# Optimization experiments

Hardware: AMD Instinct MI355X
Metric: run time of the kernel (lower is better)

Reference implementation:

```python
import jax, jax.numpy as jnp
import numpy as np
from jax import lax

N = 1024
N_I = 64
N_AV = 10
ALPHA = 0.5
RHO = 0.9
GAMMA = 1.0


def _make_params(seed=0):
    rng = np.random.RandomState(seed)
    diluition = 1.0 - N_AV / N
    W = rng.uniform(-1, 1, [N, N])
    W = W * (rng.uniform(0, 1, [N, N]) > diluition)
    eig = np.linalg.eigvals(W)
    W = (RHO * W / np.max(np.absolute(eig))).astype(np.float32)
    # N_i != 1 branch: gaussian input weights scaled by gamma
    W_in = (GAMMA * rng.randn(N_I, N)).astype(np.float32)
    return jnp.asarray(W), jnp.asarray(W_in)


def setup_inputs() -> dict:
    key = jax.random.key(0)
    Input = jax.random.normal(key, (128, N_I, 512), dtype=jnp.float32)
    W, W_in = _make_params()
    return {"Input": Input, "W": W, "W_in": W_in}


def reference(Input, W, W_in):
    # Input: [B, N_i, T] -> X: [B, N, T]
    B = Input.shape[0]
    x0 = jnp.zeros((B, W.shape[0]), dtype=Input.dtype)
    seq = jnp.transpose(Input, (2, 0, 1))  # [T, B, N_i]

    def step(x, s):
        x = (1.0 - ALPHA) * x + ALPHA * jnp.tanh(s @ W_in + x @ W)
        return x, x

    _, X = lax.scan(step, x0, seq)  # [T, B, N]
    return jnp.transpose(X, (1, 2, 0))  # [B, N, T]
```

## Files before the change

### kernel.cpp

```cpp
#include <hip/hip_runtime.h>
#include <hip/hip_fp16.h>
#include <cstdint>
#include <cstddef>

#define BB 128
#define NN 1024
#define NI 64
#define TT 512
#define MAXNNZ 16384
#define NE 28
#define TH 16

#define WS_OFFS   0u
#define WS_IDX    16384u
#define WS_VAL    65536u
#define WS_PERM   131072u
#define WS_IPERM  135168u
#define WS_XSTATE 139264u
#define WS_WINP   663552u
#define WS_EIDX2  925696u
#define WS_CNT16  983040u
#define WS_OFF16  1048576u
#define WS_U      1114112u
#define WS_U2     (WS_U + 67108864u)

__global__ __launch_bounds__(64) void k_count16(const float* __restrict__ W, int* __restrict__ cnt16) {
    int bc = blockIdx.x;
    int s = bc & 15, g = bc >> 4;
    int col = g * 64 + threadIdx.x;
    int c = 0;
    for (int q = 0; q < 64; ++q) {
        int k = s * 64 + q;
        c += (W[(size_t)k * NN + col] != 0.0f) ? 1 : 0;
    }
    cnt16[col * 16 + s] = c;
}

__global__ __launch_bounds__(1024) void k_scanrank(const int* __restrict__ cnt16,
        int* __restrict__ offs, int* __restrict__ off16,
        int* __restrict__ perm, int* __restrict__ iperm) {
    __shared__ int s[NN];
    int n = threadIdx.x;
    int t = 0;
#pragma unroll
    for (int q = 0; q < 16; ++q) t += cnt16[n * 16 + q];
    s[n] = t;
    __syncthreads();
    for (int d = 1; d < NN; d <<= 1) {
        int v = (n >= d) ? s[n - d] : 0;
        __syncthreads();
        s[n] += v;
        __syncthreads();
    }
    int incl = s[n];
    offs[n + 1] = (incl < MAXNNZ) ? incl : MAXNNZ;
    if (n == 0) offs[0] = 0;
    int base = incl - t;
#pragma unroll
    for (int q = 0; q < 16; ++q) {
        off16[n * 16 + q] = base;
        base += cnt16[n * 16 + q];
    }
    __syncthreads();
    int myc = t;
    s[n] = myc;
    __syncthreads();
    int r = 0;
    for (int m = 0; m < NN; ++m) {
        int cm = s[m];
        r += (cm > myc || (cm == myc && m < n)) ? 1 : 0;
    }
    perm[r] = n;
    iperm[n] = r;
}

__global__ __launch_bounds__(1024) void k_choice2(const int* __restrict__ offs,
        const unsigned short* __restrict__ gidx, const int* __restrict__ perm,
        const int* __restrict__ iperm, unsigned short* __restrict__ eidx2) {
    __shared__ unsigned short rk[NN][NE];
    __shared__ unsigned short scnt[NN];
    __shared__ unsigned char ctr8[896][32];
    int n = threadIdx.x;
    {
        int rr = n;
        int c = perm[rr];
        int o0 = offs[c];
        int cn = offs[c + 1] - o0;
        if (cn > NE) cn = NE;
        scnt[rr] = (unsigned short)cn;
        for (int j = 0; j < cn; ++j) rk[rr][j] = (unsigned short)iperm[(int)gidx[o0 + j]];
    }
    __syncthreads();
    int tid = n;
    if (tid < 896) {
        int task = tid >> 1, h = tid & 1;
        int w = task / NE, j = task % NE;
        unsigned char* mc = &ctr8[tid][0];
        for (int b = 0; b < 32; ++b) mc[b] = 0;
        unsigned sel = 0u;
        for (int l = 0; l < 32; ++l) {
            int rr = 64 * w + 32 * h + l;
            if (j < (int)scnt[rr]) {
                int rv = (int)rk[rr][j];
                int bA = rv & 31, bB = (rv ^ (rv >> 5)) & 31;
                if (mc[bA] <= mc[bB]) mc[bA]++;
                else { sel |= (1u << l); mc[bB]++; }
            }
        }
        for (int sweep = 0; sweep < 12; ++sweep) {
            bool ch = false;
            for (int l = 0; l < 32; ++l) {
                int rr = 64 * w + 32 * h + l;
                if (j < (int)scnt[rr]) {
                    int rv = (int)rk[rr][j];
                    int bA = rv & 31, bB = (rv ^ (rv >> 5)) & 31;
                    int isB = (int)((sel >> l) & 1u);
                    int cur = isB ? bB : bA, alt = isB ? bA : bB;
                    if ((int)mc[cur] > (int)mc[alt] + 1) {
                        mc[cur]--; mc[alt]++;
                        sel ^= (1u << l);
                        ch = true;
                    }
                }
            }
            if (!ch) break;
        }
        for (int l = 0; l < 32; ++l) {
            int rr = 64 * w + 32 * h + l;
            if (j < (int)scnt[rr]) {
                int rv = (int)rk[rr][j];
                int bB = (rv ^ (rv >> 5)) & 31;
                int addr = ((sel >> l) & 1u) ? (4096 + (((rv & ~31) | bB) << 2))
                                             : (rv << 2);
                eidx2[j * NN + rr] = (unsigned short)addr;
            }
        }
        int minb = 0, minl = (int)mc[0];
        for (int b = 1; b < 32; ++b)
            if ((int)mc[b] < minl) { minl = (int)mc[b]; minb = b; }
        unsigned short pad = (unsigned short)(minb << 2);
        for (int l = 0; l < 32; ++l) {
            int rr = 64 * w + 32 * h + l;
            if (j >= (int)scnt[rr]) eidx2[j * NN + rr] = pad;
        }
    }
}

__global__ __launch_bounds__(64) void k_fill16(const float* __restrict__ W, const int* __restrict__ off16,
                                               unsigned short* __restrict__ idx, float* __restrict__ val) {
    int bc = blockIdx.x;
    int s = bc & 15, g = bc >> 4;
    int col = g * 64 + threadIdx.x;
    int p = off16[col * 16 + s];
    for (int q = 0; q < 64; ++q) {
        int k = s * 64 + q;
        float w = W[(size_t)k * NN + col];
        if (w != 0.0f) { idx[p] = (unsigned short)k; val[p] = w; ++p; }
    }
}

__global__ __launch_bounds__(256) void k_permwin(const float* __restrict__ Win, const int* __restrict__ perm,
                                                 float* __restrict__ Winp) {
    int idx = blockIdx.x * 256 + threadIdx.x;
    int i = idx >> 10, r = idx & 1023;
    Winp[idx] = Win[(i << 10) + perm[r]];
}

__global__ __launch_bounds__(256) void k_uproj3(const float* __restrict__ In, const float* __restrict__ Winp,
                                                __half* __restrict__ U, int t0c, int nblk) {
    int b  = blockIdx.x / nblk;
    int tq = blockIdx.x % nblk;
    int t0 = t0c + tq * 32;
    __shared__ float s[32][NI + 1];
    int tid = threadIdx.x;
    {
        int i = tid >> 2, g = tid & 3;
        const float* ip = In + ((size_t)b * NI + i) * TT + t0 + g * 8;
        float4 v0 = *(const float4*)(ip);
        float4 v1 = *(const float4*)(ip + 4);
        s[g * 8 + 0][i] = v0.x; s[g * 8 + 1][i] = v0.y;
        s[g * 8 + 2][i] = v0.z; s[g * 8 + 3][i] = v0.w;
        s[g * 8 + 4][i] = v1.x; s[g * 8 + 5][i] = v1.y;
        s[g * 8 + 6][i] = v1.z; s[g * 8 + 7][i] = v1.w;
    }
    __syncthreads();
    const float4* W4 = (const float4*)Winp;
    uint2* U2 = (uint2*)U;
    for (int th = 0; th < 2; ++th) {
        float4 acc[16];
#pragma unroll
        for (int t = 0; t < 16; ++t) acc[t] = make_float4(0.f, 0.f, 0.f, 0.f);
        for (int i = 0; i < NI; ++i) {
            float4 w = W4[(size_t)i * 256 + tid];
#pragma unroll
            for (int t = 0; t < 16; ++t) {
                float sv = s[th * 16 + t][i];
                acc[t].x = fmaf(w.x, sv, acc[t].x);
                acc[t].y = fmaf(w.y, sv, acc[t].y);
                acc[t].z = fmaf(w.z, sv, acc[t].z);
                acc[t].w = fmaf(w.w, sv, acc[t].w);
            }
        }
#pragma unroll
        for (int t = 0; t < 16; ++t) {
            __half2 h01 = __floats2half2_rn(acc[t].x, acc[t].y);
            __half2 h23 = __floats2half2_rn(acc[t].z, acc[t].w);
            uint2 pk;
            pk.x = *(unsigned int*)&h01;
            pk.y = *(unsigned int*)&h23;
            U2[((size_t)(tq * 32 + th * 16 + t) * BB + b) * 256 + tid] = pk;
        }
    }
}

__device__ __forceinline__ float fast_tanh(float z) {
    float a = fabsf(z) * 2.885390082f;
    a = fminf(a, 60.0f);
    float e = __builtin_amdgcn_exp2f(a);
    float r = 1.0f - __fdividef(2.0f, e + 1.0f);
    return z < 0.0f ? -r : r;
}

#define L28(M) \
  M(0) M(1) M(2) M(3) M(4) M(5) M(6) M(7) M(8) M(9) M(10) M(11) M(12) M(13) \
  M(14) M(15) M(16) M(17) M(18) M(19) M(20) M(21) M(22) M(23) M(24) M(25) M(26) M(27)

#define DW(i)  float w##i; int a##i;
#define IW(i)  { a##i = (int)eidx2[(i) * NN + n]; \
                 w##i = (cnt > i) ? gval[o0 + i] : 0.0f; }

#define PIN_ALL \
  asm volatile("" : "+v"(w0),"+v"(w1),"+v"(w2),"+v"(w3),"+v"(w4),"+v"(w5),"+v"(w6),"+v"(w7)); \
  asm volatile("" : "+v"(w8),"+v"(w9),"+v"(w10),"+v"(w11),"+v"(w12),"+v"(w13),"+v"(w14),"+v"(w15)); \
  asm volatile("" : "+v"(w16),"+v"(w17),"+v"(w18),"+v"(w19),"+v"(w20),"+v"(w21),"+v"(w22),"+v"(w23)); \
  asm volatile("" : "+v"(w24),"+v"(w25),"+v"(w26),"+v"(w27)); \
  asm volatile("" : "+v"(a0),"+v"(a1),"+v"(a2),"+v"(a3),"+v"(a4),"+v"(a5),"+v"(a6),"+v"(a7)); \
  asm volatile("" : "+v"(a8),"+v"(a9),"+v"(a10),"+v"(a11),"+v"(a12),"+v"(a13),"+v"(a14),"+v"(a15)); \
  asm volatile("" : "+v"(a16),"+v"(a17),"+v"(a18),"+v"(a19),"+v"(a20),"+v"(a21),"+v"(a22),"+v"(a23)); \
  asm volatile("" : "+v"(a24),"+v"(a25),"+v"(a26),"+v"(a27));

#define GRP(J, i0, i1, i2, i3) \
  if ((J) < wmax) { \
    float q0 = *(const float*)(xp + a##i0); \
    float q1 = *(const float*)(xp + a##i1); \
    float q2 = *(const float*)(xp + a##i2); \
    float q3 = *(const float*)(xp + a##i3); \
    z0 = fmaf(w##i0, q0, z0); z1 = fmaf(w##i1, q1, z1); \
    z2 = fmaf(w##i2, q2, z2); z3 = fmaf(w##i3, q3, z3); \
  }

#define GATHER_ALL \
  GRP(0, 0,1,2,3)      GRP(4, 4,5,6,7)      GRP(8, 8,9,10,11) \
  GRP(12, 12,13,14,15) GRP(16, 16,17,18,19) GRP(20, 20,21,22,23) \
  GRP(24, 24,25,26,27)

#define STEP(PH, XDST) { \
    float u = un1; un1 = un2; \
    int tn = t + 2; tn = (tn < Tc) ? tn : (Tc - 1); \
    un2 = (float)Ub[(size_t)tn * ustep]; \
    const char* xp = xb + (PH); \
    float z0 = u, z1 = 0.f, z2 = 0.f, z3 = 0.f; \
    GATHER_ALL \
    x = 0.5f * x + 0.5f * fast_tanh((z0 + z1) + (z2 + z3)); \
    XDST = x; \
    float* wb = (float*)(xb + ((PH) ^ 8192)); \
    wb[n] = x; \
    wb[NN + nB] = x; \
    __syncthreads(); \
    ++t; \
}

__global__ __launch_bounds__(1024, 4)
void k_fused(const __half* __restrict__ Uread, __half* __restrict__ Uwrite,
             const float* __restrict__ In, const float* __restrict__ Winp,
             const int* __restrict__ offs, const unsigned short* __restrict__ eidx2,
             const float* __restrict__ gval, const int* __restrict__ perm,
             float* __restrict__ out, float* __restrict__ xstate,
             int t0r, int Tc, int t0u, int Tcu) {
    __shared__ float smem[4 * 32 * 65];
    int tid = threadIdx.x;
    if (blockIdx.x < BB) {
        int b = blockIdx.x, n = tid;
        int c = perm[n];
        int nB = (n & ~31) | ((n ^ (n >> 5)) & 31);
        int o0 = offs[c];
        int cnt = offs[c + 1] - o0;
        L28(DW)
        L28(IW)
        PIN_ALL
        int wmax = cnt;
#pragma unroll
        for (int d = 1; d < 64; d <<= 1) {
            int o = __shfl_xor(wmax, d);
            wmax = wmax > o ? wmax : o;
        }
        wmax = __builtin_amdgcn_readfirstlane(wmax);

        float x = (t0r == 0) ? 0.0f : xstate[((size_t)b << 10) + n];
        smem[n] = x;
        smem[NN + nB] = x;
        __syncthreads();

        char* xb = (char*)&smem[0];
        const __half* Ub = Uread + (size_t)b * NN + n;
        const size_t ustep = (size_t)BB * NN;
        float un1 = (float)Ub[0];
        float un2 = (float)Ub[(size_t)((1 < Tc) ? 1 : 0) * ustep];

        for (int tb = 0; tb < Tc; tb += TH) {
            PIN_ALL
            int t = tb;
            float y0, y1, y2, y3, y4, y5, y6, y7, y8, y9, y10, y11, y12, y13, y14, y15;
            STEP(0,    y0)
            STEP(8192, y1)
            STEP(0,    y2)
            STEP(8192, y3)
            STEP(0,    y4)
            STEP(8192, y5)
            STEP(0,    y6)
            STEP(8192, y7)
            STEP(0,    y8)
            STEP(8192, y9)
            STEP(0,    y10)
            STEP(8192, y11)
            STEP(0,    y12)
            STEP(8192, y13)
            STEP(0,    y14)
            STEP(8192, y15)
            float4* op = (float4*)(out + ((size_t)b * NN + c) * TT + (size_t)(t0r + tb));
            op[0] = make_float4(y0,  y1,  y2,  y3);
            op[1] = make_float4(y4,  y5,  y6,  y7);
            op[2] = make_float4(y8,  y9,  y10, y11);
            op[3] = make_float4(y12, y13, y14, y15);
        }
        if (t0r + Tc < TT) xstate[((size_t)b << 10) + n] = x;
    } else {
        if (Tcu <= 0) return;
        int b = blockIdx.x - BB;
        int sub = tid >> 8, stid = tid & 255;
        float* sg = smem + sub * 32 * 65;
        const float4* W4 = (const float4*)Winp;
        uint2* U2w = (uint2*)Uwrite;
        int ntile = Tcu >> 5;
        int nrep = (ntile + 3) >> 2;
        for (int rep = 0; rep < nrep; ++rep) {
            int tq = rep * 4 + sub;
            bool act = tq < ntile;
            int tg = t0u + tq * 32;
            __syncthreads();
            if (act) {
                int i = stid >> 2, g4 = stid & 3;
                const float* ip = In + ((size_t)b * NI + i) * TT + tg + g4 * 8;
                float4 v0 = *(const float4*)(ip);
                float4 v1 = *(const float4*)(ip + 4);
                sg[(g4 * 8 + 0) * 65 + i] = v0.x; sg[(g4 * 8 + 1) * 65 + i] = v0.y;
                sg[(g4 * 8 + 2) * 65 + i] = v0.z; sg[(g4 * 8 + 3) * 65 + i] = v0.w;
                sg[(g4 * 8 + 4) * 65 + i] = v1.x; sg[(g4 * 8 + 5) * 65 + i] = v1.y;
                sg[(g4 * 8 + 6) * 65 + i] = v1.z; sg[(g4 * 8 + 7) * 65 + i] = v1.w;
            }
            __syncthreads();
            if (act) {
                for (int th = 0; th < 2; ++th) {
                    float4 acc[16];
#pragma unroll
                    for (int t = 0; t < 16; ++t) acc[t] = make_float4(0.f, 0.f, 0.f, 0.f);
                    for (int i = 0; i < NI; ++i) {
                        float4 w = W4[(size_t)i * 256 + stid];
#pragma unroll
                        for (int t = 0; t < 16; ++t) {
                            float sv = sg[(th * 16 + t) * 65 + i];
                            acc[t].x = fmaf(w.x, sv, acc[t].x);
                            acc[t].y = fmaf(w.y, sv, acc[t].y);
                            acc[t].z = fmaf(w.z, sv, acc[t].z);
                            acc[t].w = fmaf(w.w, sv, acc[t].w);
                        }
                    }
#pragma unroll
                    for (int t = 0; t < 16; ++t) {
                        __half2 h01 = __floats2half2_rn(acc[t].x, acc[t].y);
                        __half2 h23 = __floats2half2_rn(acc[t].z, acc[t].w);
                        uint2 pk;
                        pk.x = *(unsigned int*)&h01;
                        pk.y = *(unsigned int*)&h23;
                        U2w[((size_t)(tq * 32 + th * 16 + t) * BB + b) * 256 + stid] = pk;
                    }
                }
            }
        }
    }
}

extern "C" void kernel_launch(void* const* d_in, const int* in_sizes, int n_in,
                              void* d_out, int out_size, void* d_ws, size_t ws_size,
                              hipStream_t stream) {
    const float* In  = (const float*)d_in[0];
    const float* W   = (const float*)d_in[1];
    const float* Win = (const float*)d_in[2];
    float* out = (float*)d_out;
    char* ws = (char*)d_ws;
    int* offs           = (int*)(ws + WS_OFFS);
    unsigned short* idx = (unsigned short*)(ws + WS_IDX);
    float* val          = (float*)(ws + WS_VAL);
    int* perm           = (int*)(ws + WS_PERM);
    int* iperm          = (int*)(ws + WS_IPERM);
    float* xstate       = (float*)(ws + WS_XSTATE);
    float* Winp         = (float*)(ws + WS_WINP);
    unsigned short* eidx2 = (unsigned short*)(ws + WS_EIDX2);
    int* cnt16          = (int*)(ws + WS_CNT16);
    int* off16          = (int*)(ws + WS_OFF16);
    __half* U0          = (__half*)(ws + WS_U);
    __half* U1          = (__half*)(ws + WS_U2);

    k_count16<<<256, 64, 0, stream>>>(W, cnt16);
    k_scanrank<<<1, 1024, 0, stream>>>(cnt16, offs, off16, perm, iperm);
    k_fill16<<<256, 64, 0, stream>>>(W, off16, idx, val);
    k_choice2<<<1, 1024, 0, stream>>>(offs, idx, perm, iperm, eidx2);
    k_permwin<<<256, 256, 0, stream>>>(Win, perm, Winp);

    if ((size_t)WS_U2 + (size_t)256 * BB * NN * 2 <= ws_size) {
        k_uproj3<<<BB, 256, 0, stream>>>(In, Winp, U0, 0, 1);
        k_fused<<<2 * BB, 1024, 0, stream>>>(U0, U1, In, Winp, offs, eidx2, val, perm,
                                             out, xstate, 0, 32, 32, 64);
        k_fused<<<2 * BB, 1024, 0, stream>>>(U1, U0, In, Winp, offs, eidx2, val, perm,
                                             out, xstate, 32, 64, 96, 128);
        k_fused<<<2 * BB, 1024, 0, stream>>>(U0, U1, In, Winp, offs, eidx2, val, perm,
                                             out, xstate, 96, 128, 224, 256);
        k_fused<<<2 * BB, 1024, 0, stream>>>(U1, U0, In, Winp, offs, eidx2, val, perm,
                                             out, xstate, 224, 256, 480, 32);
        k_fused<<<BB, 1024, 0, stream>>>(U0, U0, In, Winp, offs, eidx2, val, perm,
                                         out, xstate, 480, 32, TT, 0);
    } else {
        for (int t0 = 0; t0 < TT; t0 += 128) {
            k_uproj3<<<BB * 4, 256, 0, stream>>>(In, Winp, U0, t0, 4);
            k_fused<<<BB, 1024, 0, stream>>>(U0, U0, In, Winp, offs, eidx2, val, perm,
                                             out, xstate, t0, 128, TT, 0);
        }
    }
}
```

Baseline: 568.3 us.

## Replace multi-launch ping-pong with single persistent producer/consumer kernel using flags

Replaces the chain of five fused launches, which alternated between two U buffers, with one persistent kernel. Half the blocks compute the input projection U per 32-step tile and publish a per-batch, per-tile flag with release semantics; the other half run the recurrence, spin-waiting on each flag with acquire loads. This removes the launch boundaries and the chunked schedule, so projection and recurrence overlap continuously. It needs a full-length U buffer and relies on both block kinds being co-resident, so the spin-wait carries deadlock and occupancy risk, and the occupancy hint drops to 2 blocks per SM.

```diff
diff --git a/kernel.cpp b/kernel.cpp
--- a/kernel.cpp
+++ b/kernel.cpp
@@ -22,7 +22,6 @@
 #define WS_CNT16  983040u
 #define WS_OFF16  1048576u
 #define WS_U      1114112u
-#define WS_U2     (WS_U + 67108864u)
 
 __global__ __launch_bounds__(64) void k_count16(const float* __restrict__ W, int* __restrict__ cnt16) {
     int bc = blockIdx.x;
@@ -164,6 +163,223 @@
     int idx = blockIdx.x * 256 + threadIdx.x;
     int i = idx >> 10, r = idx & 1023;
     Winp[idx] = Win[(i << 10) + perm[r]];
+}
+
+__device__ __forceinline__ float fast_tanh(float z) {
+    float a = fabsf(z) * 2.885390082f;
+    a = fminf(a, 60.0f);
+    float e = __builtin_amdgcn_exp2f(a);
+    float r = 1.0f - __fdividef(2.0f, e + 1.0f);
+    return z < 0.0f ? -r : r;
+}
+
+#define L28(M) \
+  M(0) M(1) M(2) M(3) M(4) M(5) M(6) M(7) M(8) M(9) M(10) M(11) M(12) M(13) \
+  M(14) M(15) M(16) M(17) M(18) M(19) M(20) M(21) M(22) M(23) M(24) M(25) M(26) M(27)
+
+#define DW(i)  float w##i; int a##i;
+#define IW(i)  { a##i = (int)eidx2[(i) * NN + n]; \
+                 w##i = (cnt > i) ? gval[o0 + i] : 0.0f; }
+
+#define PIN_ALL \
+  asm volatile("" : "+v"(w0),"+v"(w1),"+v"(w2),"+v"(w3),"+v"(w4),"+v"(w5),"+v"(w6),"+v"(w7)); \
+  asm volatile("" : "+v"(w8),"+v"(w9),"+v"(w10),"+v"(w11),"+v"(w12),"+v"(w13),"+v"(w14),"+v"(w15)); \
+  asm volatile("" : "+v"(w16),"+v"(w17),"+v"(w18),"+v"(w19),"+v"(w20),"+v"(w21),"+v"(w22),"+v"(w23)); \
+  asm volatile("" : "+v"(w24),"+v"(w25),"+v"(w26),"+v"(w27)); \
+  asm volatile("" : "+v"(a0),"+v"(a1),"+v"(a2),"+v"(a3),"+v"(a4),"+v"(a5),"+v"(a6),"+v"(a7)); \
+  asm volatile("" : "+v"(a8),"+v"(a9),"+v"(a10),"+v"(a11),"+v"(a12),"+v"(a13),"+v"(a14),"+v"(a15)); \
+  asm volatile("" : "+v"(a16),"+v"(a17),"+v"(a18),"+v"(a19),"+v"(a20),"+v"(a21),"+v"(a22),"+v"(a23)); \
+  asm volatile("" : "+v"(a24),"+v"(a25),"+v"(a26),"+v"(a27));
+
+#define GRP(J, i0, i1, i2, i3) \
+  if ((J) < wmax) { \
+    float q0 = *(const float*)(xp + a##i0); \
+    float q1 = *(const float*)(xp + a##i1); \
+    float q2 = *(const float*)(xp + a##i2); \
+    float q3 = *(const float*)(xp + a##i3); \
+    z0 = fmaf(w##i0, q0, z0); z1 = fmaf(w##i1, q1, z1); \
+    z2 = fmaf(w##i2, q2, z2); z3 = fmaf(w##i3, q3, z3); \
+  }
+
+#define GATHER_ALL \
+  GRP(0, 0,1,2,3)      GRP(4, 4,5,6,7)      GRP(8, 8,9,10,11) \
+  GRP(12, 12,13,14,15) GRP(16, 16,17,18,19) GRP(20, 20,21,22,23) \
+  GRP(24, 24,25,26,27)
+
+#define STEPX(PH, XDST) { \
+    float u = un1; un1 = un2; \
+    int tn = t + 2; tn = (tn < tlim) ? tn : tlim; \
+    un2 = (float)Ub[(size_t)tn * ustep]; \
+    const char* xp = xb + (PH); \
+    float z0 = u, z1 = 0.f, z2 = 0.f, z3 = 0.f; \
+    GATHER_ALL \
+    x = 0.5f * x + 0.5f * fast_tanh((z0 + z1) + (z2 + z3)); \
+    XDST = x; \
+    float* wb = (float*)(xb + ((PH) ^ 8192)); \
+    wb[n] = x; \
+    wb[NN + nB] = x; \
+    __syncthreads(); \
+    ++t; \
+}
+
+#define REC16 \
+    PIN_ALL \
+    int t = tb; \
+    float y0, y1, y2, y3, y4, y5, y6, y7, y8, y9, y10, y11, y12, y13, y14, y15; \
+    STEPX(0,    y0)  STEPX(8192, y1)  STEPX(0,    y2)  STEPX(8192, y3) \
+    STEPX(0,    y4)  STEPX(8192, y5)  STEPX(0,    y6)  STEPX(8192, y7) \
+    STEPX(0,    y8)  STEPX(8192, y9)  STEPX(0,    y10) STEPX(8192, y11) \
+    STEPX(0,    y12) STEPX(8192, y13) STEPX(0,    y14) STEPX(8192, y15)
+
+__global__ __launch_bounds__(1024, 2)
+void k_pipe(const float* __restrict__ In, const float* __restrict__ Winp,
+            __half* __restrict__ U,
+            const int* __restrict__ offs, const unsigned short* __restrict__ eidx2,
+            const float* __restrict__ gval, const int* __restrict__ perm,
+            float* __restrict__ out, int* __restrict__ flags) {
+    __shared__ float smem[4096];
+    int tid = threadIdx.x;
+    if (blockIdx.x < BB) {
+        int b = blockIdx.x, n = tid;
+        int c = perm[n];
+        int nB = (n & ~31) | ((n ^ (n >> 5)) & 31);
+        int o0 = offs[c];
+        int cnt = offs[c + 1] - o0;
+        L28(DW)
+        L28(IW)
+        PIN_ALL
+        int wmax = cnt;
+#pragma unroll
+        for (int d = 1; d < 64; d <<= 1) {
+            int o = __shfl_xor(wmax, d);
+            wmax = wmax > o ? wmax : o;
+        }
+        wmax = __builtin_amdgcn_readfirstlane(wmax);
+
+        float x = 0.0f;
+        smem[n] = 0.0f;
+        smem[NN + nB] = 0.0f;
+        __syncthreads();
+
+        char* xb = (char*)&smem[0];
+        const __half* Ub = U + (size_t)b * NN + n;
+        const size_t ustep = (size_t)BB * NN;
+
+        for (int tile = 0; tile < 16; ++tile) {
+            if (tid == 0) {
+                while (__hip_atomic_load(&flags[b * 16 + tile], __ATOMIC_ACQUIRE,
+                                         __HIP_MEMORY_SCOPE_AGENT) == 0) {
+                    __builtin_amdgcn_s_sleep(2);
+                }
+            }
+            __syncthreads();
+            int tlim = 32 * tile + 31;
+            float un1 = (float)Ub[(size_t)(32 * tile) * ustep];
+            float un2 = (float)Ub[(size_t)(32 * tile + 1) * ustep];
+            for (int tb = 32 * tile; tb < 32 * tile + 32; tb += TH) {
+                REC16
+                float4* op = (float4*)(out + ((size_t)b * NN + c) * TT + (size_t)tb);
+                op[0] = make_float4(y0,  y1,  y2,  y3);
+                op[1] = make_float4(y4,  y5,  y6,  y7);
+                op[2] = make_float4(y8,  y9,  y10, y11);
+                op[3] = make_float4(y12, y13, y14, y15);
+            }
+        }
+    } else {
+        int b = blockIdx.x - BB;
+        int n4 = tid & 255;
+        int tl = (tid >> 8) * 8;
+        const float4* W4 = (const float4*)Winp;
+        uint2* U2w = (uint2*)U;
+        for (int tq = 0; tq < 16; ++tq) {
+            int tg = tq * 32;
+            if (tid < 512) {
+                int i = tid >> 3, g4 = tid & 7;
+                float4 v = *(const float4*)(In + ((size_t)b * NI + i) * TT + tg + g4 * 4);
+                *(float4*)&smem[i * 40 + g4 * 4] = v;
+            }
+            __syncthreads();
+            float4 a0 = {0,0,0,0}, a1 = {0,0,0,0}, a2 = {0,0,0,0}, a3 = {0,0,0,0};
+            float4 a4 = {0,0,0,0}, a5 = {0,0,0,0}, a6 = {0,0,0,0}, a7 = {0,0,0,0};
+            for (int i = 0; i < NI; ++i) {
+                float4 w = W4[(size_t)i * 256 + n4];
+                float4 sa = *(const float4*)&smem[i * 40 + tl];
+                float4 sb = *(const float4*)&smem[i * 40 + tl + 4];
+                a0.x = fmaf(w.x, sa.x, a0.x); a0.y = fmaf(w.y, sa.x, a0.y);
+                a0.z = fmaf(w.z, sa.x, a0.z); a0.w = fmaf(w.w, sa.x, a0.w);
+                a1.x = fmaf(w.x, sa.y, a1.x); a1.y = fmaf(w.y, sa.y, a1.y);
+                a1.z = fmaf(w.z, sa.y, a1.z); a1.w = fmaf(w.w, sa.y, a1.w);
+                a2.x = fmaf(w.x, sa.z, a2.x); a2.y = fmaf(w.y, sa.z, a2.y);
+                a2.z = fmaf(w.z, sa.z, a2.z); a2.w = fmaf(w.w, sa.z, a2.w);
+                a3.x = fmaf(w.x, sa.w, a3.x); a3.y = fmaf(w.y, sa.w, a3.y);
+                a3.z = fmaf(w.z, sa.w, a3.z); a3.w = fmaf(w.w, sa.w, a3.w);
+                a4.x = fmaf(w.x, sb.x, a4.x); a4.y = fmaf(w.y, sb.x, a4.y);
+                a4.z = fmaf(w.z, sb.x, a4.z); a4.w = fmaf(w.w, sb.x, a4.w);
+                a5.x = fmaf(w.x, sb.y, a5.x); a5.y = fmaf(w.y, sb.y, a5.y);
+                a5.z = fmaf(w.z, sb.y, a5.z); a5.w = fmaf(w.w, sb.y, a5.w);
+                a6.x = fmaf(w.x, sb.z, a6.x); a6.y = fmaf(w.y, sb.z, a6.y);
+                a6.z = fmaf(w.z, sb.z, a6.z); a6.w = fmaf(w.w, sb.z, a6.w);
+                a7.x = fmaf(w.x, sb.w, a7.x); a7.y = fmaf(w.y, sb.w, a7.y);
+                a7.z = fmaf(w.z, sb.w, a7.z); a7.w = fmaf(w.w, sb.w, a7.w);
+            }
+#define PSTORE(J, AJ) { \
+            int tt = tg + tl + (J); \
+            __half2 h01 = __floats2half2_rn(AJ.x, AJ.y); \
+            __half2 h23 = __floats2half2_rn(AJ.z, AJ.w); \
+            uint2 pk; pk.x = *(unsigned int*)&h01; pk.y = *(unsigned int*)&h23; \
+            U2w[((size_t)tt * BB + b) * 256 + n4] = pk; }
+            PSTORE(0, a0) PSTORE(1, a1) PSTORE(2, a2) PSTORE(3, a3)
+            PSTORE(4, a4) PSTORE(5, a5) PSTORE(6, a6) PSTORE(7, a7)
+#undef PSTORE
+            __syncthreads();
+            if (tid == 0) {
+                __hip_atomic_store(&flags[b * 16 + tq], 1, __ATOMIC_RELEASE,
+                                   __HIP_MEMORY_SCOPE_AGENT);
+            }
+        }
+    }
+}
+
+__global__ __launch_bounds__(1024, 4)
+void k_rec(const __half* __restrict__ U,
+           const int* __restrict__ offs, const unsigned short* __restrict__ eidx2,
+           const float* __restrict__ gval, const int* __restrict__ perm,
+           float* __restrict__ out, float* __restrict__ xstate, int t0r, int Tc) {
+    __shared__ float smem[4096];
+    int b = blockIdx.x, n = threadIdx.x;
+    int c = perm[n];
+    int nB = (n & ~31) | ((n ^ (n >> 5)) & 31);
+    int o0 = offs[c];
+    int cnt = offs[c + 1] - o0;
+    L28(DW)
+    L28(IW)
+    PIN_ALL
+    int wmax = cnt;
+#pragma unroll
+    for (int d = 1; d < 64; d <<= 1) {
+        int o = __shfl_xor(wmax, d);
+        wmax = wmax > o ? wmax : o;
+    }
+    wmax = __builtin_amdgcn_readfirstlane(wmax);
+    float x = (t0r == 0) ? 0.0f : xstate[((size_t)b << 10) + n];
+    smem[n] = x;
+    smem[NN + nB] = x;
+    __syncthreads();
+    char* xb = (char*)&smem[0];
+    const __half* Ub = U + (size_t)b * NN + n;
+    const size_t ustep = (size_t)BB * NN;
+    int tlim = Tc - 1;
+    float un1 = (float)Ub[0];
+    float un2 = (float)Ub[(size_t)((1 < Tc) ? 1 : 0) * ustep];
+    for (int tb = 0; tb < Tc; tb += TH) {
+        REC16
+        float4* op = (float4*)(out + ((size_t)b * NN + c) * TT + (size_t)(t0r + tb));
+        op[0] = make_float4(y0,  y1,  y2,  y3);
+        op[1] = make_float4(y4,  y5,  y6,  y7);
+        op[2] = make_float4(y8,  y9,  y10, y11);
+        op[3] = make_float4(y12, y13, y14, y15);
+    }
+    if (t0r + Tc < TT) xstate[((size_t)b << 10) + n] = x;
 }
 
 __global__ __launch_bounds__(256) void k_uproj3(const float* __restrict__ In, const float* __restrict__ Winp,
@@ -209,183 +425,6 @@
             pk.x = *(unsigned int*)&h01;
             pk.y = *(unsigned int*)&h23;
             U2[((size_t)(tq * 32 + th * 16 + t) * BB + b) * 256 + tid] = pk;
-        }
-    }
-}
-
-__device__ __forceinline__ float fast_tanh(float z) {
-    float a = fabsf(z) * 2.885390082f;
-    a = fminf(a, 60.0f);
-    float e = __builtin_amdgcn_exp2f(a);
-    float r = 1.0f - __fdividef(2.0f, e + 1.0f);
-    return z < 0.0f ? -r : r;
-}
-
-#define L28(M) \
-  M(0) M(1) M(2) M(3) M(4) M(5) M(6) M(7) M(8) M(9) M(10) M(11) M(12) M(13) \
-  M(14) M(15) M(16) M(17) M(18) M(19) M(20) M(21) M(22) M(23) M(24) M(25) M(26) M(27)
-
-#define DW(i)  float w##i; int a##i;
-#define IW(i)  { a##i = (int)eidx2[(i) * NN + n]; \
-                 w##i = (cnt > i) ? gval[o0 + i] : 0.0f; }
-
-#define PIN_ALL \
-  asm volatile("" : "+v"(w0),"+v"(w1),"+v"(w2),"+v"(w3),"+v"(w4),"+v"(w5),"+v"(w6),"+v"(w7)); \
-  asm volatile("" : "+v"(w8),"+v"(w9),"+v"(w10),"+v"(w11),"+v"(w12),"+v"(w13),"+v"(w14),"+v"(w15)); \
-  asm volatile("" : "+v"(w16),"+v"(w17),"+v"(w18),"+v"(w19),"+v"(w20),"+v"(w21),"+v"(w22),"+v"(w23)); \
-  asm volatile("" : "+v"(w24),"+v"(w25),"+v"(w26),"+v"(w27)); \
-  asm volatile("" : "+v"(a0),"+v"(a1),"+v"(a2),"+v"(a3),"+v"(a4),"+v"(a5),"+v"(a6),"+v"(a7)); \
-  asm volatile("" : "+v"(a8),"+v"(a9),"+v"(a10),"+v"(a11),"+v"(a12),"+v"(a13),"+v"(a14),"+v"(a15)); \
-  asm volatile("" : "+v"(a16),"+v"(a17),"+v"(a18),"+v"(a19),"+v"(a20),"+v"(a21),"+v"(a22),"+v"(a23)); \
-  asm volatile("" : "+v"(a24),"+v"(a25),"+v"(a26),"+v"(a27));
-
-#define GRP(J, i0, i1, i2, i3) \
-  if ((J) < wmax) { \
-    float q0 = *(const float*)(xp + a##i0); \
-    float q1 = *(const float*)(xp + a##i1); \
-    float q2 = *(const float*)(xp + a##i2); \
-    float q3 = *(const float*)(xp + a##i3); \
-    z0 = fmaf(w##i0, q0, z0); z1 = fmaf(w##i1, q1, z1); \
-    z2 = fmaf(w##i2, q2, z2); z3 = fmaf(w##i3, q3, z3); \
-  }
-
-#define GATHER_ALL \
-  GRP(0, 0,1,2,3)      GRP(4, 4,5,6,7)      GRP(8, 8,9,10,11) \
-  GRP(12, 12,13,14,15) GRP(16, 16,17,18,19) GRP(20, 20,21,22,23) \
-  GRP(24, 24,25,26,27)
-
-#define STEP(PH, XDST) { \
-    float u = un1; un1 = un2; \
-    int tn = t + 2; tn = (tn < Tc) ? tn : (Tc - 1); \
-    un2 = (float)Ub[(size_t)tn * ustep]; \
-    const char* xp = xb + (PH); \
-    float z0 = u, z1 = 0.f, z2 = 0.f, z3 = 0.f; \
-    GATHER_ALL \
-    x = 0.5f * x + 0.5f * fast_tanh((z0 + z1) + (z2 + z3)); \
-    XDST = x; \
-    float* wb = (float*)(xb + ((PH) ^ 8192)); \
-    wb[n] = x; \
-    wb[NN + nB] = x; \
-    __syncthreads(); \
-    ++t; \
-}
-
-__global__ __launch_bounds__(1024, 4)
-void k_fused(const __half* __restrict__ Uread, __half* __restrict__ Uwrite,
-             const float* __restrict__ In, const float* __restrict__ Winp,
-             const int* __restrict__ offs, const unsigned short* __restrict__ eidx2,
-             const float* __restrict__ gval, const int* __restrict__ perm,
-             float* __restrict__ out, float* __restrict__ xstate,
-             int t0r, int Tc, int t0u, int Tcu) {
-    __shared__ float smem[4 * 32 * 65];
-    int tid = threadIdx.x;
-    if (blockIdx.x < BB) {
-        int b = blockIdx.x, n = tid;
-        int c = perm[n];
-        int nB = (n & ~31) | ((n ^ (n >> 5)) & 31);
-        int o0 = offs[c];
-        int cnt = offs[c + 1] - o0;
-        L28(DW)
-        L28(IW)
-        PIN_ALL
-        int wmax = cnt;
-#pragma unroll
-        for (int d = 1; d < 64; d <<= 1) {
-            int o = __shfl_xor(wmax, d);
-            wmax = wmax > o ? wmax : o;
-        }
-        wmax = __builtin_amdgcn_readfirstlane(wmax);
-
-        float x = (t0r == 0) ? 0.0f : xstate[((size_t)b << 10) + n];
-        smem[n] = x;
-        smem[NN + nB] = x;
-        __syncthreads();
-
-        char* xb = (char*)&smem[0];
-        const __half* Ub = Uread + (size_t)b * NN + n;
-        const size_t ustep = (size_t)BB * NN;
-        float un1 = (float)Ub[0];
-        float un2 = (float)Ub[(size_t)((1 < Tc) ? 1 : 0) * ustep];
-
-        for (int tb = 0; tb < Tc; tb += TH) {
-            PIN_ALL
-            int t = tb;
-            float y0, y1, y2, y3, y4, y5, y6, y7, y8, y9, y10, y11, y12, y13, y14, y15;
-            STEP(0,    y0)
-            STEP(8192, y1)
-            STEP(0,    y2)
-            STEP(8192, y3)
-            STEP(0,    y4)
-            STEP(8192, y5)
-            STEP(0,    y6)
-            STEP(8192, y7)
-            STEP(0,    y8)
-            STEP(8192, y9)
-            STEP(0,    y10)
-            STEP(8192, y11)
-            STEP(0,    y12)
-            STEP(8192, y13)
-            STEP(0,    y14)
-            STEP(8192, y15)
-            float4* op = (float4*)(out + ((size_t)b * NN + c) * TT + (size_t)(t0r + tb));
-            op[0] = make_float4(y0,  y1,  y2,  y3);
-            op[1] = make_float4(y4,  y5,  y6,  y7);
-            op[2] = make_float4(y8,  y9,  y10, y11);
-            op[3] = make_float4(y12, y13, y14, y15);
-        }
-        if (t0r + Tc < TT) xstate[((size_t)b << 10) + n] = x;
-    } else {
-        if (Tcu <= 0) return;
-        int b = blockIdx.x - BB;
-        int sub = tid >> 8, stid = tid & 255;
-        float* sg = smem + sub * 32 * 65;
-        const float4* W4 = (const float4*)Winp;
-        uint2* U2w = (uint2*)Uwrite;
-        int ntile = Tcu >> 5;
-        int nrep = (ntile + 3) >> 2;
-        for (int rep = 0; rep < nrep; ++rep) {
-            int tq = rep * 4 + sub;
-            bool act = tq < ntile;
-            int tg = t0u + tq * 32;
-            __syncthreads();
-            if (act) {
-                int i = stid >> 2, g4 = stid & 3;
-                const float* ip = In + ((size_t)b * NI + i) * TT + tg + g4 * 8;
-                float4 v0 = *(const float4*)(ip);
-                float4 v1 = *(const float4*)(ip + 4);
-                sg[(g4 * 8 + 0) * 65 + i] = v0.x; sg[(g4 * 8 + 1) * 65 + i] = v0.y;
-                sg[(g4 * 8 + 2) * 65 + i] = v0.z; sg[(g4 * 8 + 3) * 65 + i] = v0.w;
-                sg[(g4 * 8 + 4) * 65 + i] = v1.x; sg[(g4 * 8 + 5) * 65 + i] = v1.y;
-                sg[(g4 * 8 + 6) * 65 + i] = v1.z; sg[(g4 * 8 + 7) * 65 + i] = v1.w;
-            }
-            __syncthreads();
-            if (act) {
-                for (int th = 0; th < 2; ++th) {
-                    float4 acc[16];
-#pragma unroll
-                    for (int t = 0; t < 16; ++t) acc[t] = make_float4(0.f, 0.f, 0.f, 0.f);
-                    for (int i = 0; i < NI; ++i) {
-                        float4 w = W4[(size_t)i * 256 + stid];
-#pragma unroll
-                        for (int t = 0; t < 16; ++t) {
-                            float sv = sg[(th * 16 + t) * 65 + i];
-                            acc[t].x = fmaf(w.x, sv, acc[t].x);
-                            acc[t].y = fmaf(w.y, sv, acc[t].y);
-                            acc[t].z = fmaf(w.z, sv, acc[t].z);
-                            acc[t].w = fmaf(w.w, sv, acc[t].w);
-                        }
-                    }
-#pragma unroll
-                    for (int t = 0; t < 16; ++t) {
-                        __half2 h01 = __floats2half2_rn(acc[t].x, acc[t].y);
-                        __half2 h23 = __floats2half2_rn(acc[t].z, acc[t].w);
-                        uint2 pk;
-                        pk.x = *(unsigned int*)&h01;
-                        pk.y = *(unsigned int*)&h23;
-                        U2w[((size_t)(tq * 32 + th * 16 + t) * BB + b) * 256 + stid] = pk;
-                    }
-                }
-            }
         }
     }
 }
@@ -407,33 +446,23 @@
     float* Winp         = (float*)(ws + WS_WINP);
     unsigned short* eidx2 = (unsigned short*)(ws + WS_EIDX2);
     int* cnt16          = (int*)(ws + WS_CNT16);
+    int* flags          = (int*)(ws + WS_CNT16);
     int* off16          = (int*)(ws + WS_OFF16);
-    __half* U0          = (__half*)(ws + WS_U);
-    __half* U1          = (__half*)(ws + WS_U2);
+    __half* U           = (__half*)(ws + WS_U);
 
     k_count16<<<256, 64, 0, stream>>>(W, cnt16);
     k_scanrank<<<1, 1024, 0, stream>>>(cnt16, offs, off16, perm, iperm);
+    hipMemsetAsync(flags, 0, BB * 16 * sizeof(int), stream);
     k_fill16<<<256, 64, 0, stream>>>(W, off16, idx, val);
     k_choice2<<<1, 1024, 0, stream>>>(offs, idx, perm, iperm, eidx2);
     k_permwin<<<256, 256, 0, stream>>>(Win, perm, Winp);
 
-    if ((size_t)WS_U2 + (size_t)256 * BB * NN * 2 <= ws_size) {
-        k_uproj3<<<BB, 256, 0, stream>>>(In, Winp, U0, 0, 1);
-        k_fused<<<2 * BB, 1024, 0, stream>>>(U0, U1, In, Winp, offs, eidx2, val, perm,
-                                             out, xstate, 0, 32, 32, 64);
-        k_fused<<<2 * BB, 1024, 0, stream>>>(U1, U0, In, Winp, offs, eidx2, val, perm,
-                                             out, xstate, 32, 64, 96, 128);
-        k_fused<<<2 * BB, 1024, 0, stream>>>(U0, U1, In, Winp, offs, eidx2, val, perm,
-                                             out, xstate, 96, 128, 224, 256);
-        k_fused<<<2 * BB, 1024, 0, stream>>>(U1, U0, In, Winp, offs, eidx2, val, perm,
-                                             out, xstate, 224, 256, 480, 32);
-        k_fused<<<BB, 1024, 0, stream>>>(U0, U0, In, Winp, offs, eidx2, val, perm,
-                                         out, xstate, 480, 32, TT, 0);
+    if ((size_t)WS_U + (size_t)TT * BB * NN * 2 <= ws_size) {
+        k_pipe<<<2 * BB, 1024, 0, stream>>>(In, Winp, U, offs, eidx2, val, perm, out, flags);
     } else {
         for (int t0 = 0; t0 < TT; t0 += 128) {
-            k_uproj3<<<BB * 4, 256, 0, stream>>>(In, Winp, U0, t0, 4);
-            k_fused<<<BB, 1024, 0, stream>>>(U0, U0, In, Winp, offs, eidx2, val, perm,
-                                             out, xstate, t0, 128, TT, 0);
-        }
-    }
-}
+            k_uproj3<<<BB * 4, 256, 0, stream>>>(In, Winp, U, t0, 4);
+            k_rec<<<BB, 1024, 0, stream>>>(U, offs, eidx2, val, perm, out, xstate, t0, 128);
+        }
+    }
+}
```

Result: slower. 638.6 us (+12.4%).
